# Kernel tuning notes

Measured on AMD Instinct MI355X. Metric: run time of the kernel, lower is better.

Reference implementation:

```python
import jax, jax.numpy as jnp
import numpy as np
import math

CH = 512
HEADS = 8
GROUPS = 32
EPS = 1e-5


def group_norm(x, w, b):
    # x: [B, C, T]
    B, C, T = x.shape
    xg = x.reshape(B, GROUPS, C // GROUPS, T)
    mu = xg.mean(axis=(2, 3), keepdims=True)
    var = xg.var(axis=(2, 3), keepdims=True)
    xg = (xg - mu) * jax.lax.rsqrt(var + EPS)
    return xg.reshape(B, C, T) * w[None, :, None] + b[None, :, None]


def conv1x1(x, w, b):
    # x: [B, C, T], w: [O, C, 1]
    return jnp.einsum('oc,bct->bot', w[:, :, 0], x) + b[None, :, None]


def conv3_same(x, w, b):
    y = jax.lax.conv_general_dilated(x, w, window_strides=(1,), padding='SAME',
                                     dimension_numbers=('NCH', 'OIH', 'NCH'))
    return y + b[None, :, None]


def setup_inputs() -> dict:
    key = jax.random.key(0)
    ks = jax.random.split(key, 12)
    B, Ti, Ts = 2, 4096, 1024
    inp = {
        'image': jax.random.normal(ks[0], (B, Ti, CH), jnp.float32),
        'st': jax.random.normal(ks[1], (B, Ts, CH), jnp.float32),
        'xn_w': jnp.ones((CH,), jnp.float32),
        'xn_b': jnp.zeros((CH,), jnp.float32),
        'jn_w': jnp.ones((CH,), jnp.float32),
        'jn_b': jnp.zeros((CH,), jnp.float32),
        'xqkv_w': jax.random.normal(ks[2], (3 * CH, CH, 1), jnp.float32) * (1.0 / math.sqrt(CH)),
        'xqkv_b': jnp.zeros((3 * CH,), jnp.float32),
        'jqkv_w': jax.random.normal(ks[3], (3 * CH, CH, 1), jnp.float32) * (1.0 / math.sqrt(CH)),
        'jqkv_b': jnp.zeros((3 * CH,), jnp.float32),
        # NOTE: original zero-inits proj; we use small random weights so the
        # attention path contributes to the output (same math).
        'proj_w': jax.random.normal(ks[4], (CH, CH, 3), jnp.float32) * (0.02 / math.sqrt(3 * CH)),
        'proj_b': jnp.zeros((CH,), jnp.float32),
    }
    return inp


def reference(image, st, xn_w, xn_b, jn_w, jn_b, xqkv_w, xqkv_b, jqkv_w, jqkv_b, proj_w, proj_b):
    # image: [B, Ti, C]  st: [B, Ts, C]
    x = image.transpose(0, 2, 1)           # [B, C, Ti]
    jc = st.transpose(0, 2, 1)              # [B, C, Ts]

    x_qkv = conv1x1(group_norm(x, xn_w, xn_b), xqkv_w, xqkv_b)    # [B, 3C, Ti]
    jc_qkv = conv1x1(group_norm(jc, jn_w, jn_b), jqkv_w, jqkv_b)  # [B, 3C, Ts]

    B, _, Ti = x_qkv.shape
    ch = CH // HEADS
    scale = 1.0 / math.sqrt(math.sqrt(ch))

    img_q = x_qkv[:, :CH].reshape(B, HEADS, ch, Ti)
    st_k = jc_qkv[:, CH:2 * CH].reshape(B, HEADS, ch, -1)
    st_v = jc_qkv[:, 2 * CH:].reshape(B, HEADS, ch, -1)

    # cross-attention: image queries attend to st keys/values
    w = jnp.einsum('bhct,bhcs->bhts', img_q * scale, st_k * scale)  # [B,H,Ti,Ts]
    w = jax.nn.softmax(w.astype(jnp.float32), axis=-1).astype(w.dtype)
    attn = jnp.einsum('bhts,bhcs->bhct', w, st_v).reshape(B, CH, Ti)

    x_h = conv3_same(attn, proj_w, proj_b)
    return x + x_h  # [B, C, Ti]
```

## Files before the change

kernel.cpp:

```cpp
#include <hip/hip_runtime.h>
#include <math.h>

static constexpr int CH = 512;
static constexpr int GROUPS = 32;
static constexpr int HC = 64;
static constexpr float EPS = 1e-5f;
static constexpr int TI = 4096;
static constexpr int TS = 1024;

typedef __bf16 bf16x8 __attribute__((ext_vector_type(8)));
typedef float f32x4 __attribute__((ext_vector_type(4)));

__global__ __launch_bounds__(256) void k_gn_stats(const float* __restrict__ X, int T,
                                                  float* __restrict__ stats) {
  int b = blockIdx.x >> 5;
  int g = blockIdx.x & 31;
  int tid = threadIdx.x;
  const float* base = X + ((size_t)b * T) * CH + g * 16;
  double s1 = 0.0, s2 = 0.0;
  for (int t = tid; t < T; t += 256) {
    const float4* p = (const float4*)(base + (size_t)t * CH);
#pragma unroll
    for (int q = 0; q < 4; ++q) {
      float4 v = p[q];
      s1 += (double)v.x + (double)v.y + (double)v.z + (double)v.w;
      s2 += (double)v.x * v.x + (double)v.y * v.y + (double)v.z * v.z + (double)v.w * v.w;
    }
  }
  __shared__ double r1[256];
  __shared__ double r2[256];
  r1[tid] = s1;
  r2[tid] = s2;
  __syncthreads();
  for (int s = 128; s > 0; s >>= 1) {
    if (tid < s) { r1[tid] += r1[tid + s]; r2[tid] += r2[tid + s]; }
    __syncthreads();
  }
  if (tid == 0) {
    double N = (double)16 * T;
    double mu = r1[0] / N;
    double var = r2[0] / N - mu * mu;
    float rs = (float)(1.0 / sqrt(var + (double)EPS));
    stats[(b * GROUPS + g) * 2 + 0] = (float)mu;
    stats[(b * GROUPS + g) * 2 + 1] = rs;
  }
}

__global__ __launch_bounds__(256) void k_gn_apply(const float* __restrict__ X,
                                                  const float* __restrict__ stats,
                                                  const float* __restrict__ nw,
                                                  const float* __restrict__ nb,
                                                  __bf16* __restrict__ Xp, int T) {
  size_t idx = ((size_t)blockIdx.x * 256 + threadIdx.x) * 8;
  int b = (int)(idx / ((size_t)T * 512));
  size_t rem = idx - (size_t)b * T * 512;
  int t = (int)(rem >> 9);
  int c = (int)(rem & 511);
  int g = c >> 4;
  float mu = stats[(b * GROUPS + g) * 2 + 0];
  float rs = stats[(b * GROUPS + g) * 2 + 1];
  float4 v0 = *(const float4*)(X + idx);
  float4 v1 = *(const float4*)(X + idx + 4);
  float4 w0 = *(const float4*)(nw + c);
  float4 w1 = *(const float4*)(nw + c + 4);
  float4 q0 = *(const float4*)(nb + c);
  float4 q1 = *(const float4*)(nb + c + 4);
  float xv[8] = {v0.x, v0.y, v0.z, v0.w, v1.x, v1.y, v1.z, v1.w};
  float wv[8] = {w0.x, w0.y, w0.z, w0.w, w1.x, w1.y, w1.z, w1.w};
  float qv[8] = {q0.x, q0.y, q0.z, q0.w, q1.x, q1.y, q1.z, q1.w};
  bf16x8 r;
#pragma unroll
  for (int i = 0; i < 8; ++i) {
    float a = rs * wv[i];
    r[i] = (__bf16)fmaf(xv[i], a, qv[i] - mu * a);
  }
  size_t off = ((((size_t)b * (T >> 4) + (t >> 4)) * 16 + (c >> 5)) * 64 +
                ((c >> 3) & 3) * 16 + (t & 15)) * 8;
  *(bf16x8*)(Xp + off) = r;
}

__global__ __launch_bounds__(256) void k_wpack(const float* __restrict__ W,
                                               __bf16* __restrict__ Wp) {
  int idx = blockIdx.x * 256 + threadIdx.x;
  int lane = idx & 63;
  int l = lane & 15, g = lane >> 4;
  int cb = (idx >> 6) & 15;
  int ob = idx >> 10;
  const float* src = W + (size_t)(ob * 16 + l) * 512 + cb * 32 + g * 8;
  float4 v0 = *(const float4*)src;
  float4 v1 = *(const float4*)(src + 4);
  float xv[8] = {v0.x, v0.y, v0.z, v0.w, v1.x, v1.y, v1.z, v1.w};
  bf16x8 r;
#pragma unroll
  for (int i = 0; i < 8; ++i) r[i] = (__bf16)xv[i];
  *(bf16x8*)(Wp + (size_t)idx * 8) = r;
}

__global__ __launch_bounds__(256) void k_wpack3(const float* __restrict__ W,
                                                __bf16* __restrict__ W3p) {
  int idx = blockIdx.x * 256 + threadIdx.x;
  int lane = idx & 63;
  int l = lane & 15, g = lane >> 4;
  int ob = (idx >> 6) & 31;
  int q = idx >> 11;
  int tap = q % 3;
  int cb = q / 3;
  int o = ob * 16 + l;
  int c = cb * 32 + g * 8;
  bf16x8 r;
#pragma unroll
  for (int j = 0; j < 8; ++j) r[j] = (__bf16)W[((size_t)o * 512 + c + j) * 3 + tap];
  *(bf16x8*)(W3p + (size_t)idx * 8) = r;
}

__global__ __launch_bounds__(256) void k_qkv_mfma(const __bf16* __restrict__ Xp,
                                                  const __bf16* __restrict__ Wp,
                                                  const float* __restrict__ bias,
                                                  __bf16* __restrict__ outQK,
                                                  __bf16* __restrict__ outVp,
                                                  int T) {
  int b = blockIdx.z;
  int o0 = blockIdx.y * 64;
  int tid = threadIdx.x;
  int w = tid >> 6;
  int lane = tid & 63;
  int l = lane & 15;
  int g = lane >> 4;
  int t0 = blockIdx.x * 128 + w * 32;
  int Tb = T >> 4;

  f32x4 acc[2][4] = {};
  const __bf16* Xb = Xp + (size_t)b * T * 512;

  auto load_c = [&](int cb, bf16x8 (&af)[2], bf16x8 (&wf)[4]) {
#pragma unroll
    for (int m = 0; m < 2; ++m)
      af[m] = *(const bf16x8*)(Xb + ((((size_t)(t0 >> 4) + m) * 16 + cb) * 64 + lane) * 8);
#pragma unroll
    for (int n = 0; n < 4; ++n)
      wf[n] = *(const bf16x8*)(Wp + ((((size_t)(o0 >> 4) + n) * 16 + cb) * 64 + lane) * 8);
  };
  auto mm = [&](const bf16x8 (&af)[2], const bf16x8 (&wf)[4]) {
#pragma unroll
    for (int m = 0; m < 2; ++m)
#pragma unroll
      for (int n = 0; n < 4; ++n)
        acc[m][n] = __builtin_amdgcn_mfma_f32_16x16x32_bf16(af[m], wf[n], acc[m][n], 0, 0, 0);
  };

  bf16x8 afA[2], wfA[4], afB[2], wfB[4];
  load_c(0, afA, wfA);
#pragma unroll
  for (int cb = 0; cb < 16; cb += 2) {
    load_c(cb + 1, afB, wfB);
    mm(afA, wfA);
    if (cb + 2 < 16) load_c(cb + 2, afA, wfA);
    mm(afB, wfB);
  }

  if (outVp == nullptr || o0 < 512) {
#pragma unroll
    for (int m = 0; m < 2; ++m) {
#pragma unroll
      for (int n = 0; n < 4; ++n) {
        int oo = o0 + 16 * n + l;
        float bo = bias[oo];
        int cb = oo >> 5, gp = (oo >> 3) & 3, j = oo & 7;
#pragma unroll
        for (int rr = 0; rr < 4; ++rr) {
          size_t off = ((((size_t)b * Tb + (t0 >> 4) + m) * 16 + cb) * 64 +
                        gp * 16 + 4 * g + rr) * 8 + j;
          outQK[off] = (__bf16)(acc[m][n][rr] + bo);
        }
      }
    }
  } else {
#pragma unroll
    for (int m = 0; m < 2; ++m) {
#pragma unroll
      for (int n = 0; n < 4; ++n) {
        int cb16 = ((o0 - 512) >> 4) + n;
        float bo = bias[o0 + 16 * n + l];
#pragma unroll
        for (int rr = 0; rr < 4; ++rr) {
          int sl = 16 * m + 4 * g + rr;
          size_t off = ((((size_t)b * 32 + cb16) * 32 + (t0 >> 5)) * 64 +
                        (sl >> 3) * 16 + l) * 8 + (sl & 7);
          outVp[off] = (__bf16)(acc[m][n][rr] + bo);
        }
      }
    }
  }
}

__global__ __launch_bounds__(256) void k_attn_mfma(const __bf16* __restrict__ Qp,
                                                   const __bf16* __restrict__ Kp,
                                                   const __bf16* __restrict__ Vp,
                                                   __bf16* __restrict__ outA) {
  int b = blockIdx.z;
  int h = blockIdx.y;
  int tid = threadIdx.x;
  int w = tid >> 6;
  int lane = tid & 63;
  int l = lane & 15;
  int g = lane >> 4;
  int t0 = blockIdx.x * 128 + w * 32;

  __shared__ __align__(16) __bf16 Plds[4][32][72];

  bf16x8 qf[2][2];
#pragma unroll
  for (int m = 0; m < 2; ++m)
#pragma unroll
    for (int ks = 0; ks < 2; ++ks)
      qf[m][ks] = *(const bf16x8*)(Qp + ((((size_t)b * 256 + (t0 >> 4) + m) * 16 +
                                          2 * h + ks) * 64 + lane) * 8);

  f32x4 o_acc[2][4] = {};
  float l_run[2][4] = {};
  bf16x8 kfA[4][2], kfB[4][2], vf[4][2];

  auto load_k = [&](int s0, bf16x8 (&kf)[4][2]) {
#pragma unroll
    for (int n = 0; n < 4; ++n)
#pragma unroll
      for (int ks = 0; ks < 2; ++ks)
        kf[n][ks] = *(const bf16x8*)(Kp + ((((size_t)b * 64 + (s0 >> 4) + n) * 16 +
                                            2 * h + ks) * 64 + lane) * 8);
  };
  auto load_v = [&](int s0) {
#pragma unroll
    for (int n = 0; n < 4; ++n)
#pragma unroll
      for (int ks = 0; ks < 2; ++ks)
        vf[n][ks] = *(const bf16x8*)(Vp + ((((size_t)b * 32 + h * 4 + n) * 32 +
                                            (s0 >> 5) + ks) * 64 + lane) * 8);
  };
  auto tile = [&](const bf16x8 (&kf)[4][2]) {
    f32x4 s_acc[2][4];
#pragma unroll
    for (int m = 0; m < 2; ++m)
#pragma unroll
      for (int n = 0; n < 4; ++n) {
        f32x4 z = {0.f, 0.f, 0.f, 0.f};
        z = __builtin_amdgcn_mfma_f32_16x16x32_bf16(qf[m][0], kf[n][0], z, 0, 0, 0);
        s_acc[m][n] = __builtin_amdgcn_mfma_f32_16x16x32_bf16(qf[m][1], kf[n][1], z, 0, 0, 0);
      }
#pragma unroll
    for (int m = 0; m < 2; ++m) {
      float rs_[4] = {0.f, 0.f, 0.f, 0.f};
#pragma unroll
      for (int n = 0; n < 4; ++n) {
#pragma unroll
        for (int r = 0; r < 4; ++r) {
          float p = __expf(s_acc[m][n][r] * 0.125f);
          s_acc[m][n][r] = p;
          rs_[r] += p;
          Plds[w][16 * m + 4 * g + r][16 * n + l] = (__bf16)p;
        }
      }
#pragma unroll
      for (int r = 0; r < 4; ++r) {
        float v = rs_[r];
#pragma unroll
        for (int mm = 1; mm < 16; mm <<= 1) v += __shfl_xor(v, mm, 64);
        l_run[m][r] += v;
      }
    }
    bf16x8 pa[2][2];
#pragma unroll
    for (int m = 0; m < 2; ++m)
#pragma unroll
      for (int ks = 0; ks < 2; ++ks)
        pa[m][ks] = *(const bf16x8*)&Plds[w][16 * m + l][32 * ks + 8 * g];
#pragma unroll
    for (int m = 0; m < 2; ++m)
#pragma unroll
      for (int n = 0; n < 4; ++n) {
        o_acc[m][n] = __builtin_amdgcn_mfma_f32_16x16x32_bf16(pa[m][0], vf[n][0], o_acc[m][n], 0, 0, 0);
        o_acc[m][n] = __builtin_amdgcn_mfma_f32_16x16x32_bf16(pa[m][1], vf[n][1], o_acc[m][n], 0, 0, 0);
      }
  };

  load_k(0, kfA);
#pragma unroll 1
  for (int s0 = 0; s0 < TS; s0 += 128) {
    load_v(s0);
    load_k(s0 + 64, kfB);
    tile(kfA);
    load_v(s0 + 64);
    if (s0 + 128 < TS) load_k(s0 + 128, kfA);
    tile(kfB);
  }

  float inv[2][4];
#pragma unroll
  for (int m = 0; m < 2; ++m)
#pragma unroll
    for (int r = 0; r < 4; ++r) inv[m][r] = 1.f / l_run[m][r];
#pragma unroll
  for (int m = 0; m < 2; ++m)
#pragma unroll
    for (int n = 0; n < 4; ++n)
#pragma unroll
      for (int r = 0; r < 4; ++r)
        Plds[w][16 * m + 4 * g + r][16 * n + l] = (__bf16)(o_acc[m][n][r] * inv[m][r]);
  int row = lane & 31, half = lane >> 5;
#pragma unroll
  for (int k = 0; k < 4; ++k) {
    bf16x8 v = *(const bf16x8*)&Plds[w][row][half * 32 + k * 8];
    *(bf16x8*)(outA + ((size_t)b * TI + t0 + row) * 512 + h * 64 + half * 32 + k * 8) = v;
  }
}

__global__ __launch_bounds__(256) void k_conv3_mfma(const __bf16* __restrict__ A,
                                                    const __bf16* __restrict__ W3p,
                                                    const float* __restrict__ bias,
                                                    const float* __restrict__ image,
                                                    float* __restrict__ out) {
  int b = blockIdx.z;
  int o0 = blockIdx.y * 64;
  int ob0 = o0 >> 4;
  int tid = threadIdx.x;
  int w = tid >> 6;
  int lane = tid & 63;
  int l = lane & 15;
  int g = lane >> 4;
  int t0 = blockIdx.x * 128;
  int t0w = t0 + w * 32;

  __shared__ __align__(16) __bf16 Alds[2][130 * 32];
  __shared__ __align__(16) __bf16 Wlds[2][12 * 512];

  const __bf16* Ab = A + (size_t)b * TI * 512;

  auto stage = [&](int cb, int buf) {
#pragma unroll
    for (int pass = 0; pass < 3; ++pass) {
      int gi = tid + pass * 256;
      if (gi < 520) {
        int r = gi >> 2, gg = gi & 3;
        int t = t0 - 1 + r;
        bf16x8 v = {};
        if (t >= 0 && t < TI) v = *(const bf16x8*)(Ab + (size_t)t * 512 + cb * 32 + gg * 8);
        *(bf16x8*)&Alds[buf][r * 32 + ((gg ^ (r & 3)) << 3)] = v;
      }
    }
#pragma unroll
    for (int ch = w; ch < 12; ch += 4) {
      bf16x8 v = *(const bf16x8*)(W3p + ((((size_t)cb * 3 + (ch >> 2)) * 32 + ob0 +
                                          (ch & 3)) * 64 + lane) * 8);
      *(bf16x8*)&Wlds[buf][ch * 512 + lane * 8] = v;
    }
  };

  f32x4 acc[2][4] = {};

  stage(0, 0);
  __syncthreads();
#pragma unroll 1
  for (int cs = 0; cs < 16; ++cs) {
    int cur = cs & 1;
    if (cs < 15) stage(cs + 1, cur ^ 1);
    bf16x8 af[3][2], wf[3][4];
#pragma unroll
    for (int tap = 0; tap < 3; ++tap) {
#pragma unroll
      for (int m = 0; m < 2; ++m) {
        int r = w * 32 + 16 * m + l + tap;
        af[tap][m] = *(const bf16x8*)&Alds[cur][r * 32 + ((g ^ (r & 3)) << 3)];
      }
#pragma unroll
      for (int n = 0; n < 4; ++n)
        wf[tap][n] = *(const bf16x8*)&Wlds[cur][(tap * 4 + n) * 512 + lane * 8];
    }
#pragma unroll
    for (int tap = 0; tap < 3; ++tap)
#pragma unroll
      for (int m = 0; m < 2; ++m)
#pragma unroll
        for (int n = 0; n < 4; ++n)
          acc[m][n] =
              __builtin_amdgcn_mfma_f32_16x16x32_bf16(af[tap][m], wf[tap][n], acc[m][n], 0, 0, 0);
    __syncthreads();
  }

#pragma unroll
  for (int m = 0; m < 2; ++m) {
    int tb = t0w + 16 * m + 4 * g;
#pragma unroll
    for (int n = 0; n < 4; ++n) {
      int o = o0 + 16 * n + l;
      float bo = bias[o];
      f32x4 r;
#pragma unroll
      for (int rr = 0; rr < 4; ++rr)
        r[rr] = acc[m][n][rr] + bo + image[((size_t)b * TI + tb + rr) * CH + o];
      *(f32x4*)(out + ((size_t)b * CH + o) * TI + tb) = r;
    }
  }
}

extern "C" void kernel_launch(void* const* d_in, const int* in_sizes, int n_in,
                              void* d_out, int out_size, void* d_ws, size_t ws_size,
                              hipStream_t stream) {
  const float* image = (const float*)d_in[0];
  const float* st = (const float*)d_in[1];
  const float* xn_w = (const float*)d_in[2];
  const float* xn_b = (const float*)d_in[3];
  const float* jn_w = (const float*)d_in[4];
  const float* jn_b = (const float*)d_in[5];
  const float* xqkv_w = (const float*)d_in[6];
  const float* xqkv_b = (const float*)d_in[7];
  const float* jqkv_w = (const float*)d_in[8];
  const float* jqkv_b = (const float*)d_in[9];
  const float* proj_w = (const float*)d_in[10];
  const float* proj_b = (const float*)d_in[11];
  float* out = (float*)d_out;
  float* ws = (float*)d_ws;

  float* stats_x = ws;
  float* stats_j = ws + 128;
  __bf16* Xnp = (__bf16*)(ws + 256);
  __bf16* abuf = Xnp;
  __bf16* stnp = Xnp + (size_t)2 * TI * CH;
  __bf16* wqb = stnp + (size_t)2 * TS * CH;
  __bf16* wkvb = wqb + (size_t)CH * CH;
  __bf16* wb3 = wkvb + (size_t)2 * CH * CH;
  __bf16* Qp = wb3 + (size_t)3 * CH * CH;
  __bf16* Kp = Qp + (size_t)2 * TI * CH;
  __bf16* Vp = Kp + (size_t)2 * TS * CH;

  k_gn_stats<<<dim3(64), dim3(256), 0, stream>>>(image, TI, stats_x);
  k_gn_stats<<<dim3(64), dim3(256), 0, stream>>>(st, TS, stats_j);

  k_gn_apply<<<dim3(2 * TI * 512 / 2048), dim3(256), 0, stream>>>(image, stats_x, xn_w, xn_b, Xnp, TI);
  k_gn_apply<<<dim3(2 * TS * 512 / 2048), dim3(256), 0, stream>>>(st, stats_j, jn_w, jn_b, stnp, TS);

  k_wpack<<<dim3(128), dim3(256), 0, stream>>>(xqkv_w, wqb);
  k_wpack<<<dim3(256), dim3(256), 0, stream>>>(jqkv_w + (size_t)CH * CH, wkvb);
  k_wpack3<<<dim3(384), dim3(256), 0, stream>>>(proj_w, wb3);

  k_qkv_mfma<<<dim3(TI / 128, CH / 64, 2), dim3(256), 0, stream>>>(
      Xnp, wqb, xqkv_b, Qp, nullptr, TI);
  k_qkv_mfma<<<dim3(TS / 128, 1024 / 64, 2), dim3(256), 0, stream>>>(
      stnp, wkvb, jqkv_b + CH, Kp, Vp, TS);

  k_attn_mfma<<<dim3(TI / 128, 8, 2), dim3(256), 0, stream>>>(Qp, Kp, Vp, abuf);

  k_conv3_mfma<<<dim3(TI / 128, CH / 64, 2), dim3(256), 0, stream>>>(
      abuf, wb3, proj_b, image, out);
}
```

Measured before the change: 141.7 us.

## Split attention key range across two waves and fold softmax scale into Q

```diff
diff --git a/kernel.cpp b/kernel.cpp
--- a/kernel.cpp
+++ b/kernel.cpp
@@ -158,7 +158,23 @@
     mm(afB, wfB);
   }
 
-  if (outVp == nullptr || o0 < 512) {
+  if (outVp == nullptr) {
+#pragma unroll
+    for (int m = 0; m < 2; ++m) {
+#pragma unroll
+      for (int n = 0; n < 4; ++n) {
+        int oo = o0 + 16 * n + l;
+        float bo = bias[oo];
+        int cb = oo >> 5, gp = (oo >> 3) & 3, j = oo & 7;
+#pragma unroll
+        for (int rr = 0; rr < 4; ++rr) {
+          size_t off = ((((size_t)b * Tb + (t0 >> 4) + m) * 16 + cb) * 64 +
+                        gp * 16 + 4 * g + rr) * 8 + j;
+          outQK[off] = (__bf16)((acc[m][n][rr] + bo) * 0.125f);
+        }
+      }
+    }
+  } else if (o0 < 512) {
 #pragma unroll
     for (int m = 0; m < 2; ++m) {
 #pragma unroll
@@ -193,10 +209,10 @@
   }
 }
 
-__global__ __launch_bounds__(256) void k_attn_mfma(const __bf16* __restrict__ Qp,
-                                                   const __bf16* __restrict__ Kp,
-                                                   const __bf16* __restrict__ Vp,
-                                                   __bf16* __restrict__ outA) {
+__global__ __launch_bounds__(128, 4) void k_attn_mfma(const __bf16* __restrict__ Qp,
+                                                      const __bf16* __restrict__ Kp,
+                                                      const __bf16* __restrict__ Vp,
+                                                      __bf16* __restrict__ outA) {
   int b = blockIdx.z;
   int h = blockIdx.y;
   int tid = threadIdx.x;
@@ -204,9 +220,11 @@
   int lane = tid & 63;
   int l = lane & 15;
   int g = lane >> 4;
-  int t0 = blockIdx.x * 128 + w * 32;
-
-  __shared__ __align__(16) __bf16 Plds[4][32][72];
+  int t0 = blockIdx.x * 32;
+
+  __shared__ __align__(16) __bf16 Plds[2][32][72];
+  __shared__ float Ored[64][32];
+  __shared__ float Lred[64][8];
 
   bf16x8 qf[2][2];
 #pragma unroll
@@ -217,26 +235,25 @@
                                           2 * h + ks) * 64 + lane) * 8);
 
   f32x4 o_acc[2][4] = {};
-  float l_run[2][4] = {};
-  bf16x8 kfA[4][2], kfB[4][2], vf[4][2];
-
-  auto load_k = [&](int s0, bf16x8 (&kf)[4][2]) {
+  float rs_acc[2][4] = {};
+
+  int s_base = w * 512;
+#pragma unroll 1
+  for (int s0 = s_base; s0 < s_base + 512; s0 += 64) {
+    bf16x8 kf[4][2];
 #pragma unroll
     for (int n = 0; n < 4; ++n)
 #pragma unroll
       for (int ks = 0; ks < 2; ++ks)
         kf[n][ks] = *(const bf16x8*)(Kp + ((((size_t)b * 64 + (s0 >> 4) + n) * 16 +
                                             2 * h + ks) * 64 + lane) * 8);
-  };
-  auto load_v = [&](int s0) {
+    bf16x8 vf[4][2];
 #pragma unroll
     for (int n = 0; n < 4; ++n)
 #pragma unroll
       for (int ks = 0; ks < 2; ++ks)
         vf[n][ks] = *(const bf16x8*)(Vp + ((((size_t)b * 32 + h * 4 + n) * 32 +
                                             (s0 >> 5) + ks) * 64 + lane) * 8);
-  };
-  auto tile = [&](const bf16x8 (&kf)[4][2]) {
     f32x4 s_acc[2][4];
 #pragma unroll
     for (int m = 0; m < 2; ++m)
@@ -247,26 +264,15 @@
         s_acc[m][n] = __builtin_amdgcn_mfma_f32_16x16x32_bf16(qf[m][1], kf[n][1], z, 0, 0, 0);
       }
 #pragma unroll
-    for (int m = 0; m < 2; ++m) {
-      float rs_[4] = {0.f, 0.f, 0.f, 0.f};
-#pragma unroll
-      for (int n = 0; n < 4; ++n) {
+    for (int m = 0; m < 2; ++m)
+#pragma unroll
+      for (int n = 0; n < 4; ++n)
 #pragma unroll
         for (int r = 0; r < 4; ++r) {
-          float p = __expf(s_acc[m][n][r] * 0.125f);
-          s_acc[m][n][r] = p;
-          rs_[r] += p;
+          float p = __expf(s_acc[m][n][r]);
+          rs_acc[m][r] += p;
           Plds[w][16 * m + 4 * g + r][16 * n + l] = (__bf16)p;
         }
-      }
-#pragma unroll
-      for (int r = 0; r < 4; ++r) {
-        float v = rs_[r];
-#pragma unroll
-        for (int mm = 1; mm < 16; mm <<= 1) v += __shfl_xor(v, mm, 64);
-        l_run[m][r] += v;
-      }
-    }
     bf16x8 pa[2][2];
 #pragma unroll
     for (int m = 0; m < 2; ++m)
@@ -280,36 +286,51 @@
         o_acc[m][n] = __builtin_amdgcn_mfma_f32_16x16x32_bf16(pa[m][0], vf[n][0], o_acc[m][n], 0, 0, 0);
         o_acc[m][n] = __builtin_amdgcn_mfma_f32_16x16x32_bf16(pa[m][1], vf[n][1], o_acc[m][n], 0, 0, 0);
       }
-  };
-
-  load_k(0, kfA);
-#pragma unroll 1
-  for (int s0 = 0; s0 < TS; s0 += 128) {
-    load_v(s0);
-    load_k(s0 + 64, kfB);
-    tile(kfA);
-    load_v(s0 + 64);
-    if (s0 + 128 < TS) load_k(s0 + 128, kfA);
-    tile(kfB);
-  }
-
-  float inv[2][4];
-#pragma unroll
-  for (int m = 0; m < 2; ++m)
-#pragma unroll
-    for (int r = 0; r < 4; ++r) inv[m][r] = 1.f / l_run[m][r];
-#pragma unroll
-  for (int m = 0; m < 2; ++m)
-#pragma unroll
-    for (int n = 0; n < 4; ++n)
-#pragma unroll
-      for (int r = 0; r < 4; ++r)
-        Plds[w][16 * m + 4 * g + r][16 * n + l] = (__bf16)(o_acc[m][n][r] * inv[m][r]);
-  int row = lane & 31, half = lane >> 5;
-#pragma unroll
-  for (int k = 0; k < 4; ++k) {
-    bf16x8 v = *(const bf16x8*)&Plds[w][row][half * 32 + k * 8];
-    *(bf16x8*)(outA + ((size_t)b * TI + t0 + row) * 512 + h * 64 + half * 32 + k * 8) = v;
+  }
+
+  if (w == 1) {
+#pragma unroll
+    for (int m = 0; m < 2; ++m)
+#pragma unroll
+      for (int n = 0; n < 4; ++n)
+#pragma unroll
+        for (int r = 0; r < 4; ++r) Ored[lane][m * 16 + n * 4 + r] = o_acc[m][n][r];
+#pragma unroll
+    for (int m = 0; m < 2; ++m)
+#pragma unroll
+      for (int r = 0; r < 4; ++r) Lred[lane][m * 4 + r] = rs_acc[m][r];
+  }
+  __syncthreads();
+  if (w == 0) {
+#pragma unroll
+    for (int m = 0; m < 2; ++m)
+#pragma unroll
+      for (int n = 0; n < 4; ++n)
+#pragma unroll
+        for (int r = 0; r < 4; ++r) o_acc[m][n][r] += Ored[lane][m * 16 + n * 4 + r];
+    float inv[2][4];
+#pragma unroll
+    for (int m = 0; m < 2; ++m)
+#pragma unroll
+      for (int r = 0; r < 4; ++r) {
+        float v = rs_acc[m][r] + Lred[lane][m * 4 + r];
+#pragma unroll
+        for (int mm = 1; mm < 16; mm <<= 1) v += __shfl_xor(v, mm, 64);
+        inv[m][r] = 1.f / v;
+      }
+#pragma unroll
+    for (int m = 0; m < 2; ++m)
+#pragma unroll
+      for (int n = 0; n < 4; ++n)
+#pragma unroll
+        for (int r = 0; r < 4; ++r)
+          Plds[0][16 * m + 4 * g + r][16 * n + l] = (__bf16)(o_acc[m][n][r] * inv[m][r]);
+    int row = lane & 31, half = lane >> 5;
+#pragma unroll
+    for (int k = 0; k < 4; ++k) {
+      bf16x8 v = *(const bf16x8*)&Plds[0][row][half * 32 + k * 8];
+      *(bf16x8*)(outA + ((size_t)b * TI + t0 + row) * 512 + h * 64 + half * 32 + k * 8) = v;
+    }
   }
 }
 
@@ -446,7 +467,7 @@
   k_qkv_mfma<<<dim3(TS / 128, 1024 / 64, 2), dim3(256), 0, stream>>>(
       stnp, wkvb, jqkv_b + CH, Kp, Vp, TS);
 
-  k_attn_mfma<<<dim3(TI / 128, 8, 2), dim3(256), 0, stream>>>(Qp, Kp, Vp, abuf);
+  k_attn_mfma<<<dim3(TI / 32, 8, 2), dim3(128), 0, stream>>>(Qp, Kp, Vp, abuf);
 
   k_conv3_mfma<<<dim3(TI / 128, CH / 64, 2), dim3(256), 0, stream>>>(
       abuf, wb3, proj_b, image, out);
```

Result: faster. 134.3 us (-5.2%).
